# Kernel tuning notes

Measured on AMD Instinct MI355X. Metric: run time of the kernel, lower is better.

## Reference

```python
import jax, jax.numpy as jnp
import numpy as np

B, N, D = 4, 2048, 2048
HEADS, KV_HEADS = 16, 4
DH = D // HEADS            # 128 per-head dim
KV_RATIO = HEADS // KV_HEADS
MAX_LEN, MAX_BSZ = 2048, 4
EPS = 1.1920929e-07        # torch.finfo(float32).eps (RMSNorm default eps=None)


def _rot_tables(n, d, base=10000.0):
    thetas = base ** (-jnp.arange(0, d, 2, dtype=jnp.float32) / d)   # [d/2]
    ang = jnp.arange(n, dtype=jnp.float32)[:, None] * thetas[None, :]
    cos = jnp.repeat(jnp.cos(ang), 2, axis=-1)   # [n, d] interleaved pairs
    sin = jnp.repeat(jnp.sin(ang), 2, axis=-1)
    return cos, sin


def _rotate_half_inverted(x):
    x1 = x[..., ::2]
    x2 = x[..., 1::2]
    return jnp.stack([-x2, x1], axis=-1).reshape(x.shape)


def _apply_rotation(x, end, start=0):
    cos, sin = _rot_tables(MAX_LEN, DH)
    return x * cos[start:end] + _rotate_half_inverted(x) * sin[start:end]


def setup_inputs() -> dict:
    key = jax.random.key(0)
    ks = jax.random.split(key, 4)
    s = 0.02
    return {
        "x": jax.random.normal(ks[0], (B, N, D), jnp.float32),
        "norm_w": jnp.ones((D,), jnp.float32),
        "qw": jax.random.normal(ks[1], (HEADS * DH, D), jnp.float32) * s,
        "qb": jnp.zeros((HEADS * DH,), jnp.float32),
        "kvw": jax.random.normal(ks[2], (2 * DH * KV_HEADS, D), jnp.float32) * s,
        "kvb": jnp.zeros((2 * DH * KV_HEADS,), jnp.float32),
        "wow": jax.random.normal(ks[3], (D, HEADS * DH), jnp.float32) * s,
        "wob": jnp.zeros((D,), jnp.float32),
        "kv_cache": jnp.zeros((MAX_BSZ, MAX_LEN, 2 * DH * KV_HEADS), jnp.float32),
        "pos": 0,
    }


def reference(x, norm_w, qw, qb, kvw, kvb, wow, wob, kv_cache, pos):
    b, n, d = x.shape
    t = pos + n  # total cached length
    # RMSNorm
    xn = x * jax.lax.rsqrt(jnp.mean(x * x, axis=-1, keepdims=True) + EPS) * norm_w
    # Q projection -> [b, heads, n, dh]
    q = (xn @ qw.T + qb).reshape(b, n, HEADS, DH).transpose(0, 2, 1, 3)
    # KV projection + cache write/read
    kv = xn @ kvw.T + kvb                                  # [b, n, 2*dh*kv_heads]
    cache = jax.lax.dynamic_update_slice(kv_cache, kv, (0, pos, 0))
    kvf = cache[:b, :t].reshape(b, t, KV_HEADS, 2 * DH).transpose(0, 2, 1, 3)
    kvf = jnp.repeat(kvf, KV_RATIO, axis=1)                # GQA expand -> [b, heads, t, 2dh]
    k, v = kvf[..., :DH], kvf[..., DH:]
    # RoPE (interleaved-pair variant)
    q = _apply_rotation(q, t, pos)
    k = _apply_rotation(k, t, 0)
    # Attention (decoder causal)
    attn = jnp.einsum("bhqd,bhkd->bhqk", q, k) / jnp.sqrt(jnp.float32(DH))
    if n > 1:
        mask = jnp.triu(jnp.ones((n, t), bool), k=1 + pos)
        attn = jnp.where(mask, -jnp.inf, attn)
    attn = jax.nn.softmax(attn, axis=-1)
    o = jnp.einsum("bhqk,bhkd->bhqd", attn, v).transpose(0, 2, 1, 3).reshape(b, n, HEADS * DH)
    return o @ wow.T + wob
```

## Files before the change

kernel.cpp:

```cpp
#include <hip/hip_runtime.h>
#include <hip/hip_bf16.h>

typedef unsigned short u16;
typedef unsigned int u32;
typedef __attribute__((ext_vector_type(4))) float f32x4;
typedef __attribute__((ext_vector_type(8))) short s16x8;

#define B_ 4
#define N_ 2048
#define D_ 2048
#define HEADS_ 16
#define KVH_ 4
#define DH_ 128
#define KVD_ 1024
#define M_ 8192
#define QSCALE2_ 0.12753257518622628f

__device__ __forceinline__ u16 f2bf(float f) {
  u32 u = __builtin_bit_cast(u32, f);
  return (u16)((u + 0x7FFFu + ((u >> 16) & 1u)) >> 16);
}

__device__ __forceinline__ float fexp2(float x) {
#if __has_builtin(__builtin_amdgcn_exp2f)
  return __builtin_amdgcn_exp2f(x);
#else
  return exp2f(x);
#endif
}

__device__ __forceinline__ void gload_lds16(const void* g, void* l) {
  __builtin_amdgcn_global_load_lds(
      (const __attribute__((address_space(1))) u32*)g,
      (__attribute__((address_space(3))) u32*)l, 16, 0, 0);
}

__global__ __launch_bounds__(256)
void rope_tab_k(float* __restrict__ cost, float* __restrict__ sint)
{
  const int idx = blockIdx.x * 256 + threadIdx.x;
  const int p = idx >> 6, i = idx & 63;
  const float theta = expf(-(float)i * 0.015625f * 9.210340371976184f);
  float s, c;
  sincosf((float)p * theta, &s, &c);
  cost[idx] = c;
  sint[idx] = s;
}

__global__ __launch_bounds__(256)
void cvt_bf16_k(const float* __restrict__ s, u16* __restrict__ d, int n)
{
  const int i = (blockIdx.x * 256 + threadIdx.x) * 8;
  if (i >= n) return;
  const f32x4 a = *(const f32x4*)(s + i);
  const f32x4 b = *(const f32x4*)(s + i + 4);
  s16x8 o;
  #pragma unroll
  for (int j = 0; j < 4; ++j) { o[j] = (short)f2bf(a[j]); o[4 + j] = (short)f2bf(b[j]); }
  *(s16x8*)(d + i) = o;
}

__global__ __launch_bounds__(256)
void rmsnorm_k(const float* __restrict__ x, const float* __restrict__ w, u16* __restrict__ xn)
{
  const int row = blockIdx.x, t = threadIdx.x;
  const float* xr = x + (size_t)row * D_;
  const f32x4 a = *(const f32x4*)(xr + t * 8);
  const f32x4 b = *(const f32x4*)(xr + t * 8 + 4);
  float ss = a[0]*a[0] + a[1]*a[1] + a[2]*a[2] + a[3]*a[3]
           + b[0]*b[0] + b[1]*b[1] + b[2]*b[2] + b[3]*b[3];
  #pragma unroll
  for (int off = 32; off >= 1; off >>= 1) ss += __shfl_xor(ss, off);
  __shared__ float wss[4];
  if ((t & 63) == 0) wss[t >> 6] = ss;
  __syncthreads();
  const float tot = wss[0] + wss[1] + wss[2] + wss[3];
  const float rs = rsqrtf(tot * (1.0f / D_) + 1.1920929e-07f);
  s16x8 o;
  #pragma unroll
  for (int j = 0; j < 4; ++j) {
    o[j]     = (short)f2bf(a[j] * rs * w[t * 8 + j]);
    o[4 + j] = (short)f2bf(b[j] * rs * w[t * 8 + 4 + j]);
  }
  *(s16x8*)(xn + (size_t)row * D_ + t * 8) = o;
}

template<int EPI>
__global__ __launch_bounds__(512, 2)
void gemm_p(const u16* __restrict__ A, const u16* __restrict__ Bw,
            void* __restrict__ Cv, void* __restrict__ Cv2,
            const float* __restrict__ bias, const float* __restrict__ bias2,
            const float* __restrict__ cos_t, const float* __restrict__ sin_t)
{
  __shared__ __align__(16) u16 As[2][8192];
  __shared__ __align__(16) u16 Bs[2][4096];
  const int t = threadIdx.x, w = t >> 6, l = t & 63;
  const int g = l >> 4, lr = l & 15;
  const int wm = w >> 2, wn = w & 3;

  const int nbx = gridDim.x;
  const int nb = nbx * gridDim.y;
  const int flat = blockIdx.y * nbx + blockIdx.x;
  const int swz = (flat & 7) * (nb >> 3) + (flat >> 3);
  const int row0 = (swz / nbx) * 256, col0 = (swz % nbx) * 128;

  const int NT = 64;

  const int srow = w * 16 + (l >> 2);
  const int scol = (l & 3) * 8;
  const u16* gA = A + (size_t)(row0 + srow) * 2048 + scol;
  const u16* gB = Bw + (size_t)(col0 + srow) * 2048 + scol;

  f32x4 acc[8][2] = {};

  auto stage_tile = [&](int kt2, int pb) {
    gload_lds16(gA + (size_t)kt2 * 32, &As[pb][(w * 16) * 32]);
    gload_lds16(gA + (size_t)128 * 2048 + kt2 * 32, &As[pb][(128 + w * 16) * 32]);
    gload_lds16(gB + (size_t)kt2 * 32, &Bs[pb][(w * 16) * 32]);
  };

  stage_tile(0, 0);

  for (int kt = 0; kt < NT; ++kt) {
    const int p = kt & 1;
    if (kt + 1 < NT) {
      stage_tile(kt + 1, p ^ 1);
      asm volatile("s_waitcnt vmcnt(3)" ::: "memory");
    } else {
      asm volatile("s_waitcnt vmcnt(0)" ::: "memory");
    }
    __builtin_amdgcn_s_barrier();

    s16x8 bf[2], af[8];
    #pragma unroll
    for (int nf = 0; nf < 2; ++nf)
      bf[nf] = *(const s16x8*)(&Bs[p][(wn * 32 + nf * 16 + lr) * 32 + g * 8]);
    #pragma unroll
    for (int mf = 0; mf < 8; ++mf)
      af[mf] = *(const s16x8*)(&As[p][(wm * 128 + mf * 16 + lr) * 32 + g * 8]);

    __builtin_amdgcn_s_setprio(1);
    #pragma unroll
    for (int mf = 0; mf < 8; ++mf)
      #pragma unroll
      for (int nf = 0; nf < 2; ++nf)
        acc[mf][nf] = __builtin_amdgcn_mfma_f32_16x16x32_bf16(af[mf], bf[nf], acc[mf][nf], 0, 0, 0);
    __builtin_amdgcn_s_setprio(0);
    __builtin_amdgcn_sched_barrier(0);
    __builtin_amdgcn_s_barrier();
  }

  #pragma unroll
  for (int mf = 0; mf < 8; ++mf) {
    #pragma unroll
    for (int nf = 0; nf < 2; ++nf) {
      const int cc = col0 + wn * 32 + nf * 16 + lr;
      const float bv = (EPI == 4 && cc >= 2048) ? bias2[cc - 2048] : bias[cc];
      #pragma unroll
      for (int j = 0; j < 4; ++j) {
        const int rr = row0 + wm * 128 + mf * 16 + g * 4 + j;
        float v = acc[mf][nf][j] + bv;
        if (EPI == 0) {
          ((float*)Cv)[(size_t)rr * 2048 + cc] = v;
        } else {
          const int pos = rr & (N_ - 1);
          const float pv = __shfl_xor(v, 1);
          if (cc < 2048) {
            const int d = cc & (DH_ - 1);
            const float c = cos_t[pos * 64 + (d >> 1)];
            const float s = sin_t[pos * 64 + (d >> 1)];
            const float o = (cc & 1) ? fmaf(v, c, pv * s) : fmaf(v, c, -pv * s);
            ((u16*)Cv)[(size_t)rr * 2048 + cc] = f2bf(o);
          } else {
            const int ccc = cc - 2048;
            const int dm = ccc & 255;
            float o = v;
            if (dm < DH_) {
              const float c = cos_t[pos * 64 + (dm >> 1)];
              const float s = sin_t[pos * 64 + (dm >> 1)];
              o = (dm & 1) ? fmaf(v, c, pv * s) : fmaf(v, c, -pv * s);
            }
            ((u16*)Cv2)[(size_t)rr * 1024 + ccc] = f2bf(o);
          }
        }
      }
    }
  }
}

__global__ __launch_bounds__(256)
void vtrans_k(const u16* __restrict__ kvb, u16* __restrict__ vt)
{
  __shared__ u16 tile[64][65];
  const int z = blockIdx.z, b = z >> 2, kh = z & 3;
  const int p0 = blockIdx.x * 64, d0 = blockIdx.y * 64;
  const int t = threadIdx.x;
  #pragma unroll
  for (int r = 0; r < 2; ++r) {
    const int pl = r * 32 + (t >> 3), dl = (t & 7) * 8;
    const s16x8 v = *(const s16x8*)(kvb + (size_t)(b * N_ + p0 + pl) * KVD_ + kh * 256 + 128 + d0 + dl);
    #pragma unroll
    for (int jj = 0; jj < 8; ++jj) tile[pl][dl + jj] = (u16)v[jj];
  }
  __syncthreads();
  #pragma unroll
  for (int r = 0; r < 2; ++r) {
    const int dl = r * 32 + (t >> 3), pl = (t & 7) * 8;
    s16x8 o;
    #pragma unroll
    for (int jj = 0; jj < 8; ++jj) o[jj] = (short)tile[pl + jj][dl];
    *(s16x8*)(vt + ((size_t)(z * DH_ + d0 + dl)) * N_ + p0 + pl) = o;
  }
}

__global__ __launch_bounds__(512, 2)
void attn_k(const u16* __restrict__ q, const u16* __restrict__ kvb,
            const u16* __restrict__ vt, u16* __restrict__ out)
{
  const int fi = blockIdx.x, h = blockIdx.y, b = blockIdx.z;
  const int kh = h >> 2;
  const int t = threadIdx.x, w = t >> 6, lane = t & 63;
  const int g = lane >> 4, lr = lane & 15;

  __shared__ __align__(16) u16 Ks[2][64 * 128];
  __shared__ __align__(16) u16 Vs[2][128 * 64];
  __shared__ __align__(16) u16 Ps[8][16 * 64];

  const int kc = 2 * w;
  const int kr0 = kc * 4 + (lane >> 4);
  const int ksw0 = (lane & 15) ^ (kr0 & 7);
  const int kr1 = kr0 + 4;
  const int ksw1 = (lane & 15) ^ (kr1 & 7);
  const int vd0 = kc * 8 + (lane >> 3);
  const int vsw0 = (lane & 7) ^ (vd0 & 7);
  const int vd1 = vd0 + 8;
  const int vsw1 = (lane & 7) ^ (vd1 & 7);

  const u16* kbase = kvb + (size_t)b * (N_ * KVD_) + kh * 256;
  const u16* vbase = vt + (size_t)((b * KVH_ + kh) * DH_) * N_;

  int cur = 0;

  auto issue = [&](int kt, int buf) {
    gload_lds16(kbase + (size_t)(kt * 64 + kr0) * KVD_ + ksw0 * 8, &Ks[buf][kc * 512]);
    gload_lds16(kbase + (size_t)(kt * 64 + kr1) * KVD_ + ksw1 * 8, &Ks[buf][(kc + 1) * 512]);
    gload_lds16(vbase + (size_t)vd0 * N_ + kt * 64 + vsw0 * 8, &Vs[buf][kc * 512]);
    gload_lds16(vbase + (size_t)vd1 * N_ + kt * 64 + vsw1 * 8, &Vs[buf][(kc + 1) * 512]);
  };

  auto run_qtile = [&](int qi, int nkt, bool chain) {
    const int qrow0 = qi * 128 + w * 16;
    const int td = qrow0 >> 6;
    s16x8 qf[4];
    {
      const u16* qp = q + (size_t)(b * N_ + qrow0 + lr) * D_ + h * DH_;
      #pragma unroll
      for (int ks = 0; ks < 4; ++ks) qf[ks] = *(const s16x8*)(qp + ks * 32 + g * 8);
    }
    f32x4 o_acc[8] = {};
    float m_j[4], l_j[4];
    #pragma unroll
    for (int j = 0; j < 4; ++j) { m_j[j] = -1e30f; l_j[j] = 0.0f; }

    for (int kt = 0; kt < nkt; ++kt) {
      __syncthreads();
      if (kt + 1 < nkt)      issue(kt + 1, cur ^ 1);
      else if (chain)        issue(0, cur ^ 1);

      if (kt <= td) {
        const u16* Kc = &Ks[cur][0];
        const u16* Vc = &Vs[cur][0];

        f32x4 sf[4] = {};
        __builtin_amdgcn_s_setprio(1);
        #pragma unroll
        for (int ks = 0; ks < 4; ++ks) {
          #pragma unroll
          for (int kvf = 0; kvf < 4; ++kvf) {
            const int kvr = kvf * 16 + lr;
            const int ba = (kvr * 256 + ks * 64 + g * 16) ^ ((kvr & 7) << 4);
            const s16x8 kf = *(const s16x8*)((const char*)Kc + ba);
            sf[kvf] = __builtin_amdgcn_mfma_f32_16x16x32_bf16(qf[ks], kf, sf[kvf], 0, 0, 0);
          }
        }
        __builtin_amdgcn_s_setprio(0);

        const bool need_mask = (kt == td);
        float pmax[4];
        #pragma unroll
        for (int j = 0; j < 4; ++j) {
          float mx = -1e30f;
          #pragma unroll
          for (int kvf = 0; kvf < 4; ++kvf) {
            float sv = sf[kvf][j] * QSCALE2_;
            if (need_mask) {
              const int kj = kt * 64 + kvf * 16 + lr;
              const int qi_row = qrow0 + g * 4 + j;
              if (kj > qi_row) sv = -1e30f;
            }
            sf[kvf][j] = sv;
            mx = fmaxf(mx, sv);
          }
          mx = fmaxf(mx, __shfl_xor(mx, 1));
          mx = fmaxf(mx, __shfl_xor(mx, 2));
          mx = fmaxf(mx, __shfl_xor(mx, 4));
          mx = fmaxf(mx, __shfl_xor(mx, 8));
          pmax[j] = mx;
        }

        const float needv = fmaxf(fmaxf(pmax[0] - m_j[0], pmax[1] - m_j[1]),
                                  fmaxf(pmax[2] - m_j[2], pmax[3] - m_j[3]));
        if (__any(needv > 8.0f)) {
          #pragma unroll
          for (int j = 0; j < 4; ++j) {
            const float mn = fmaxf(m_j[j], pmax[j]);
            const float pf = fexp2(m_j[j] - mn);
            m_j[j] = mn;
            l_j[j] *= pf;
            #pragma unroll
            for (int df = 0; df < 8; ++df) o_acc[df][j] *= pf;
          }
        }

        #pragma unroll
        for (int j = 0; j < 4; ++j) {
          float lacc = 0.0f;
          #pragma unroll
          for (int kvf = 0; kvf < 4; ++kvf) {
            const float p = fexp2(sf[kvf][j] - m_j[j]);
            lacc += p;
            const int rq = g * 4 + j, ck = kvf * 16 + lr;
            const int ba = (rq * 128 + ck * 2) ^ ((rq & 7) << 4);
            *(u16*)((char*)&Ps[w][0] + ba) = (u16)(__builtin_bit_cast(u32, p) >> 16);
          }
          l_j[j] += lacc;
        }

        __builtin_amdgcn_s_setprio(1);
        #pragma unroll
        for (int kk = 0; kk < 2; ++kk) {
          const int bap = (lr * 128 + kk * 64 + g * 16) ^ ((lr & 7) << 4);
          const s16x8 pf = *(const s16x8*)((const char*)&Ps[w][0] + bap);
          #pragma unroll
          for (int df = 0; df < 8; ++df) {
            const int dd = df * 16 + lr;
            const int bav = (dd * 128 + kk * 64 + g * 16) ^ ((dd & 7) << 4);
            const s16x8 vf = *(const s16x8*)((const char*)Vc + bav);
            o_acc[df] = __builtin_amdgcn_mfma_f32_16x16x32_bf16(pf, vf, o_acc[df], 0, 0, 0);
          }
        }
        __builtin_amdgcn_s_setprio(0);
      }
      cur ^= 1;
    }

    float inv_l[4];
    #pragma unroll
    for (int j = 0; j < 4; ++j) {
      float s4 = l_j[j];
      s4 += __shfl_xor(s4, 1);
      s4 += __shfl_xor(s4, 2);
      s4 += __shfl_xor(s4, 4);
      s4 += __shfl_xor(s4, 8);
      inv_l[j] = 1.0f / s4;
    }
    u16* op = out + (size_t)(b * N_ + qrow0) * D_ + h * DH_;
    #pragma unroll
    for (int df = 0; df < 8; ++df)
      #pragma unroll
      for (int j = 0; j < 4; ++j)
        op[(size_t)(g * 4 + j) * D_ + df * 16 + lr] = f2bf(o_acc[df][j] * inv_l[j]);
  };

  const int qlo = fi, qhi = 15 - fi;
  issue(0, 0);
  run_qtile(qlo, 2 * qlo + 2, true);
  run_qtile(qhi, 2 * qhi + 2, false);
}

extern "C" void kernel_launch(void* const* d_in, const int* in_sizes, int n_in,
                              void* d_out, int out_size, void* d_ws, size_t ws_size,
                              hipStream_t stream) {
  const float* x      = (const float*)d_in[0];
  const float* normw  = (const float*)d_in[1];
  const float* qw     = (const float*)d_in[2];
  const float* qbias  = (const float*)d_in[3];
  const float* kvw    = (const float*)d_in[4];
  const float* kvbias = (const float*)d_in[5];
  const float* wow    = (const float*)d_in[6];
  const float* wob    = (const float*)d_in[7];
  float* out = (float*)d_out;

  char* ws = (char*)d_ws;
  u16* xn    = (u16*)(ws + 0);
  u16* dq    = (u16*)(ws + 33554432);
  u16* dkv   = (u16*)(ws + 67108864);
  u16* dvt   = (u16*)(ws + 83886080);
  u16* wqkv  = (u16*)(ws + 92274688);
  u16* wowb  = (u16*)(ws + 104857600);
  float* cost = (float*)(ws + 113246208);
  float* sint = (float*)(ws + 113770496);

  rope_tab_k<<<512, 256, 0, stream>>>(cost, sint);
  cvt_bf16_k<<<2048, 256, 0, stream>>>(qw, wqkv, 2048 * 2048);
  cvt_bf16_k<<<1024, 256, 0, stream>>>(kvw, wqkv + 2048 * 2048, 1024 * 2048);
  cvt_bf16_k<<<2048, 256, 0, stream>>>(wow, wowb, 2048 * 2048);
  rmsnorm_k<<<8192, 256, 0, stream>>>(x, normw, xn);
  gemm_p<4><<<dim3(24, 32), 512, 0, stream>>>(xn, wqkv, (void*)dq, (void*)dkv,
                                              qbias, kvbias, cost, sint);
  vtrans_k<<<dim3(32, 2, 16), 256, 0, stream>>>(dkv, dvt);
  attn_k<<<dim3(8, 16, 4), 512, 0, stream>>>(dq, dkv, dvt, xn);
  gemm_p<0><<<dim3(16, 32), 512, 0, stream>>>(xn, wowb, (void*)out, nullptr,
                                              wob, nullptr, nullptr, nullptr);
}
```

Measured before the change: 423.1 us.

## Double attention query tile per wave to reuse K/V fragments across two row blocks

```diff
diff --git a/kernel.cpp b/kernel.cpp
--- a/kernel.cpp
+++ b/kernel.cpp
@@ -213,7 +213,7 @@
   }
 }
 
-__global__ __launch_bounds__(512, 2)
+__global__ __launch_bounds__(512, 1)
 void attn_k(const u16* __restrict__ q, const u16* __restrict__ kvb,
             const u16* __restrict__ vt, u16* __restrict__ out)
 {
@@ -224,7 +224,7 @@
 
   __shared__ __align__(16) u16 Ks[2][64 * 128];
   __shared__ __align__(16) u16 Vs[2][128 * 64];
-  __shared__ __align__(16) u16 Ps[8][16 * 64];
+  __shared__ __align__(16) u16 Ps[8][32 * 64];
 
   const int kc = 2 * w;
   const int kr0 = kc * 4 + (lane >> 4);
@@ -249,18 +249,21 @@
   };
 
   auto run_qtile = [&](int qi, int nkt, bool chain) {
-    const int qrow0 = qi * 128 + w * 16;
-    const int td = qrow0 >> 6;
-    s16x8 qf[4];
-    {
-      const u16* qp = q + (size_t)(b * N_ + qrow0 + lr) * D_ + h * DH_;
-      #pragma unroll
-      for (int ks = 0; ks < 4; ++ks) qf[ks] = *(const s16x8*)(qp + ks * 32 + g * 8);
+    const int qrow0 = qi * 256 + w * 32;
+    const int td = (qrow0 + 31) >> 6;
+    s16x8 qf[2][4];
+    #pragma unroll
+    for (int r = 0; r < 2; ++r) {
+      const u16* qp = q + (size_t)(b * N_ + qrow0 + r * 16 + lr) * D_ + h * DH_;
+      #pragma unroll
+      for (int ks = 0; ks < 4; ++ks) qf[r][ks] = *(const s16x8*)(qp + ks * 32 + g * 8);
     }
-    f32x4 o_acc[8] = {};
-    float m_j[4], l_j[4];
-    #pragma unroll
-    for (int j = 0; j < 4; ++j) { m_j[j] = -1e30f; l_j[j] = 0.0f; }
+    f32x4 o_acc[2][8] = {};
+    float m_j[2][4], l_j[2][4];
+    #pragma unroll
+    for (int r = 0; r < 2; ++r)
+      #pragma unroll
+      for (int j = 0; j < 4; ++j) { m_j[r][j] = -1e30f; l_j[r][j] = 0.0f; }
 
     for (int kt = 0; kt < nkt; ++kt) {
       __syncthreads();
@@ -271,7 +274,7 @@
         const u16* Kc = &Ks[cur][0];
         const u16* Vc = &Vs[cur][0];
 
-        f32x4 sf[4] = {};
+        f32x4 sf[2][4] = {};
         __builtin_amdgcn_s_setprio(1);
         #pragma unroll
         for (int ks = 0; ks < 4; ++ks) {
@@ -280,73 +283,91 @@
             const int kvr = kvf * 16 + lr;
             const int ba = (kvr * 256 + ks * 64 + g * 16) ^ ((kvr & 7) << 4);
             const s16x8 kf = *(const s16x8*)((const char*)Kc + ba);
-            sf[kvf] = __builtin_amdgcn_mfma_f32_16x16x32_bf16(qf[ks], kf, sf[kvf], 0, 0, 0);
+            sf[0][kvf] = __builtin_amdgcn_mfma_f32_16x16x32_bf16(qf[0][ks], kf, sf[0][kvf], 0, 0, 0);
+            sf[1][kvf] = __builtin_amdgcn_mfma_f32_16x16x32_bf16(qf[1][ks], kf, sf[1][kvf], 0, 0, 0);
           }
         }
         __builtin_amdgcn_s_setprio(0);
 
         const bool need_mask = (kt == td);
-        float pmax[4];
-        #pragma unroll
-        for (int j = 0; j < 4; ++j) {
-          float mx = -1e30f;
-          #pragma unroll
-          for (int kvf = 0; kvf < 4; ++kvf) {
-            float sv = sf[kvf][j] * QSCALE2_;
-            if (need_mask) {
-              const int kj = kt * 64 + kvf * 16 + lr;
-              const int qi_row = qrow0 + g * 4 + j;
-              if (kj > qi_row) sv = -1e30f;
+        float pmax[2][4];
+        #pragma unroll
+        for (int r = 0; r < 2; ++r) {
+          #pragma unroll
+          for (int j = 0; j < 4; ++j) {
+            float mx = -1e30f;
+            #pragma unroll
+            for (int kvf = 0; kvf < 4; ++kvf) {
+              float sv = sf[r][kvf][j] * QSCALE2_;
+              if (need_mask) {
+                const int kj = kt * 64 + kvf * 16 + lr;
+                const int qi_row = qrow0 + r * 16 + g * 4 + j;
+                if (kj > qi_row) sv = -1e30f;
+              }
+              sf[r][kvf][j] = sv;
+              mx = fmaxf(mx, sv);
             }
-            sf[kvf][j] = sv;
-            mx = fmaxf(mx, sv);
-          }
-          mx = fmaxf(mx, __shfl_xor(mx, 1));
-          mx = fmaxf(mx, __shfl_xor(mx, 2));
-          mx = fmaxf(mx, __shfl_xor(mx, 4));
-          mx = fmaxf(mx, __shfl_xor(mx, 8));
-          pmax[j] = mx;
-        }
-
-        const float needv = fmaxf(fmaxf(pmax[0] - m_j[0], pmax[1] - m_j[1]),
-                                  fmaxf(pmax[2] - m_j[2], pmax[3] - m_j[3]));
+            mx = fmaxf(mx, __shfl_xor(mx, 1));
+            mx = fmaxf(mx, __shfl_xor(mx, 2));
+            mx = fmaxf(mx, __shfl_xor(mx, 4));
+            mx = fmaxf(mx, __shfl_xor(mx, 8));
+            pmax[r][j] = mx;
+          }
+        }
+
+        float needv = -1e30f;
+        #pragma unroll
+        for (int r = 0; r < 2; ++r)
+          #pragma unroll
+          for (int j = 0; j < 4; ++j) needv = fmaxf(needv, pmax[r][j] - m_j[r][j]);
         if (__any(needv > 8.0f)) {
           #pragma unroll
+          for (int r = 0; r < 2; ++r)
+            #pragma unroll
+            for (int j = 0; j < 4; ++j) {
+              const float mn = fmaxf(m_j[r][j], pmax[r][j]);
+              const float pf = fexp2(m_j[r][j] - mn);
+              m_j[r][j] = mn;
+              l_j[r][j] *= pf;
+              #pragma unroll
+              for (int df = 0; df < 8; ++df) o_acc[r][df][j] *= pf;
+            }
+        }
+
+        #pragma unroll
+        for (int r = 0; r < 2; ++r) {
+          #pragma unroll
           for (int j = 0; j < 4; ++j) {
-            const float mn = fmaxf(m_j[j], pmax[j]);
-            const float pf = fexp2(m_j[j] - mn);
-            m_j[j] = mn;
-            l_j[j] *= pf;
+            float lacc = 0.0f;
             #pragma unroll
-            for (int df = 0; df < 8; ++df) o_acc[df][j] *= pf;
-          }
-        }
-
-        #pragma unroll
-        for (int j = 0; j < 4; ++j) {
-          float lacc = 0.0f;
-          #pragma unroll
-          for (int kvf = 0; kvf < 4; ++kvf) {
-            const float p = fexp2(sf[kvf][j] - m_j[j]);
-            lacc += p;
-            const int rq = g * 4 + j, ck = kvf * 16 + lr;
-            const int ba = (rq * 128 + ck * 2) ^ ((rq & 7) << 4);
-            *(u16*)((char*)&Ps[w][0] + ba) = (u16)(__builtin_bit_cast(u32, p) >> 16);
-          }
-          l_j[j] += lacc;
+            for (int kvf = 0; kvf < 4; ++kvf) {
+              const float p = fexp2(sf[r][kvf][j] - m_j[r][j]);
+              lacc += p;
+              const int rq = r * 16 + g * 4 + j, ck = kvf * 16 + lr;
+              const int ba = (rq * 128 + ck * 2) ^ ((rq & 7) << 4);
+              *(u16*)((char*)&Ps[w][0] + ba) = (u16)(__builtin_bit_cast(u32, p) >> 16);
+            }
+            l_j[r][j] += lacc;
+          }
         }
 
         __builtin_amdgcn_s_setprio(1);
         #pragma unroll
         for (int kk = 0; kk < 2; ++kk) {
-          const int bap = (lr * 128 + kk * 64 + g * 16) ^ ((lr & 7) << 4);
-          const s16x8 pf = *(const s16x8*)((const char*)&Ps[w][0] + bap);
+          s16x8 pf[2];
+          #pragma unroll
+          for (int r = 0; r < 2; ++r) {
+            const int prow = r * 16 + lr;
+            const int bap = (prow * 128 + kk * 64 + g * 16) ^ ((prow & 7) << 4);
+            pf[r] = *(const s16x8*)((const char*)&Ps[w][0] + bap);
+          }
           #pragma unroll
           for (int df = 0; df < 8; ++df) {
             const int dd = df * 16 + lr;
             const int bav = (dd * 128 + kk * 64 + g * 16) ^ ((dd & 7) << 4);
             const s16x8 vf = *(const s16x8*)((const char*)Vc + bav);
-            o_acc[df] = __builtin_amdgcn_mfma_f32_16x16x32_bf16(pf, vf, o_acc[df], 0, 0, 0);
+            o_acc[0][df] = __builtin_amdgcn_mfma_f32_16x16x32_bf16(pf[0], vf, o_acc[0][df], 0, 0, 0);
+            o_acc[1][df] = __builtin_amdgcn_mfma_f32_16x16x32_bf16(pf[1], vf, o_acc[1][df], 0, 0, 0);
           }
         }
         __builtin_amdgcn_s_setprio(0);
@@ -354,28 +375,31 @@
       cur ^= 1;
     }
 
-    float inv_l[4];
-    #pragma unroll
-    for (int j = 0; j < 4; ++j) {
-      float s4 = l_j[j];
-      s4 += __shfl_xor(s4, 1);
-      s4 += __shfl_xor(s4, 2);
-      s4 += __shfl_xor(s4, 4);
-      s4 += __shfl_xor(s4, 8);
-      inv_l[j] = 1.0f / s4;
+    #pragma unroll
+    for (int r = 0; r < 2; ++r) {
+      float inv_l[4];
+      #pragma unroll
+      for (int j = 0; j < 4; ++j) {
+        float s4 = l_j[r][j];
+        s4 += __shfl_xor(s4, 1);
+        s4 += __shfl_xor(s4, 2);
+        s4 += __shfl_xor(s4, 4);
+        s4 += __shfl_xor(s4, 8);
+        inv_l[j] = 1.0f / s4;
+      }
+      u16* op = out + (size_t)(b * N_ + qrow0 + r * 16) * D_ + h * DH_;
+      #pragma unroll
+      for (int df = 0; df < 8; ++df)
+        #pragma unroll
+        for (int j = 0; j < 4; ++j)
+          op[(size_t)(g * 4 + j) * D_ + df * 16 + lr] = f2bf(o_acc[r][df][j] * inv_l[j]);
     }
-    u16* op = out + (size_t)(b * N_ + qrow0) * D_ + h * DH_;
-    #pragma unroll
-    for (int df = 0; df < 8; ++df)
-      #pragma unroll
-      for (int j = 0; j < 4; ++j)
-        op[(size_t)(g * 4 + j) * D_ + df * 16 + lr] = f2bf(o_acc[df][j] * inv_l[j]);
   };
 
-  const int qlo = fi, qhi = 15 - fi;
+  const int qlo = fi, qhi = 7 - fi;
   issue(0, 0);
-  run_qtile(qlo, 2 * qlo + 2, true);
-  run_qtile(qhi, 2 * qhi + 2, false);
+  run_qtile(qlo, 4 * qlo + 4, true);
+  run_qtile(qhi, 4 * qhi + 4, false);
 }
 
 extern "C" void kernel_launch(void* const* d_in, const int* in_sizes, int n_in,
@@ -409,7 +433,7 @@
   gemm_p<4><<<dim3(24, 32), 512, 0, stream>>>(xn, wqkv, (void*)dq, (void*)dkv,
                                               qbias, kvbias, cost, sint);
   vtrans_k<<<dim3(32, 2, 16), 256, 0, stream>>>(dkv, dvt);
-  attn_k<<<dim3(8, 16, 4), 512, 0, stream>>>(dq, dkv, dvt, xn);
+  attn_k<<<dim3(4, 16, 4), 512, 0, stream>>>(dq, dkv, dvt, xn);
   gemm_p<0><<<dim3(16, 32), 512, 0, stream>>>(xn, wowb, (void*)out, nullptr,
                                               wob, nullptr, nullptr, nullptr);
 }
```

New measurement: 408.9 us. 3.4% less time.
